# Kernel tuning notes

Measured on AMD Instinct MI355X. Metric: run time of the kernel, lower is better.

The kernel has to match this reference:

```python
import jax, jax.numpy as jnp
import numpy as np

CV_CHAN = 49  # displacement channels; radius = (CV_CHAN - 1) // 2 = 24


def conv1x1(x, W, b):
    # x: [B,C,H,Wd], W: [O,C], b: [O] -> [B,O,H,Wd]
    return jnp.einsum('oc,bchw->bohw', W, x) + b[None, :, None, None]


def corr_volume(f1, f2, radius, eps):
    """Shift-and-dot correlation along width. f1,f2: [B,C,H,W] -> [B,2r+1,H,W].
    Channel k corresponds to displacement d = k - radius; out-of-range positions are 0
    (handled by zero-padding, matching the torch zero-filled shifted tensors)."""
    f1n = f1 / (jnp.linalg.norm(f1, axis=1, keepdims=True) + eps)
    f2n = f2 / (jnp.linalg.norm(f2, axis=1, keepdims=True) + eps)
    Wd = f1.shape[3]
    pad = jnp.pad(f2n, ((0, 0), (0, 0), (0, 0), (radius, radius)))
    # shifted_k[x] = f2n[x - d] = pad[x + 2*radius - k]
    slices = [
        jnp.sum(f1n * jax.lax.dynamic_slice_in_dim(pad, 2 * radius - k, Wd, axis=3), axis=1)
        for k in range(2 * radius + 1)
    ]
    return jnp.stack(slices, axis=1)


def setup_inputs() -> dict:
    key = jax.random.key(0)
    ks = jax.random.split(key, 10)
    B, C, H, W = 4, 128, 128, 256
    F = 128  # fmap channels
    G = 96   # geo encoder output channels
    s = 0.05
    return {
        'feat_l1': jax.random.normal(ks[0], (B, C, H, W), jnp.float32),
        'feat_r1': jax.random.normal(ks[1], (B, C, H, W), jnp.float32),
        'cv0': jax.random.normal(ks[2], (B, CV_CHAN, H, W), jnp.float32),
        'cv1': jax.random.normal(ks[3], (B, CV_CHAN, H, W), jnp.float32),
        'cv2': jax.random.normal(ks[4], (B, CV_CHAN, H, W), jnp.float32),
        'W_f1': jax.random.normal(ks[5], (F, C), jnp.float32) * s,
        'b_f1': jnp.zeros((F,), jnp.float32),
        'W_f2': jax.random.normal(ks[6], (F, C), jnp.float32) * s,
        'b_f2': jnp.zeros((F,), jnp.float32),
        'W_geo': jax.random.normal(ks[7], (G, CV_CHAN), jnp.float32) * s,
        'b_geo': jnp.zeros((G,), jnp.float32),
        'W_sel': jax.random.normal(ks[8], (3, 3 * G), jnp.float32) * s,
        'b_sel': jnp.zeros((3,), jnp.float32),
    }


def reference(feat_l1, feat_r1, cv0, cv1, cv2,
              W_f1, b_f1, W_f2, b_f2, W_geo, b_geo, W_sel, b_sel):
    # init feature maps (init_fmap1 / init_fmap2 as 1x1 convs)
    fmap1 = conv1x1(feat_l1, W_f1, b_f1)
    fmap2 = conv1x1(feat_r1, W_f2, b_f2)
    radius = (CV_CHAN - 1) // 2
    init_corr = corr_volume(fmap1, fmap2, radius, 1e-8)  # [B, CV_CHAN, H, W]

    # geo_volume2 (1x1 conv CV_CHAN -> 96) applied to each geometric volume
    g0 = conv1x1(cv0, W_geo, b_geo)
    g1 = conv1x1(cv1, W_geo, b_geo)
    g2 = conv1x1(cv2, W_geo, b_geo)
    combined_g = jnp.concatenate([g0, g1, g2], axis=1)  # [B, 288, H, W]

    logits = conv1x1(combined_g, W_sel, b_sel)           # [B, 3, H, W]
    w = jax.nn.softmax(logits, axis=1)

    weighted = (w[:, 0:1] * cv0[:, :CV_CHAN]
                + w[:, 1:2] * cv1[:, :CV_CHAN]
                + w[:, 2:3] * cv2[:, :CV_CHAN])
    final = init_corr + weighted
    return (final, init_corr, w)
```

## Files before the change

kernel.cpp:

```cpp
#include <hip/hip_runtime.h>

#define HW 32768
#define WIDTH 256

typedef float f32x4 __attribute__((ext_vector_type(4)));
typedef short s16x8 __attribute__((ext_vector_type(8)));

__device__ __forceinline__ unsigned short f2bf(float f){
    unsigned int u = __float_as_uint(f);
    u += 0x7FFFu + ((u >> 16) & 1u);
    return (unsigned short)(u >> 16);
}
__device__ __forceinline__ unsigned int pk2(float a, float b){
    return (unsigned int)f2bf(a) | ((unsigned int)f2bf(b) << 16);
}

__global__ void k_pre(const float* __restrict__ W1, const float* __restrict__ W2,
                      unsigned int* __restrict__ Wb,
                      const float* __restrict__ Wsel, const float* __restrict__ bsel,
                      const float* __restrict__ Wgeo, const float* __restrict__ bgeo,
                      float* __restrict__ M, float* __restrict__ c0)
{
    if (blockIdx.x < 64){
        const int pi = blockIdx.x * 256 + threadIdx.x;
        const int j2   = pi & 3;
        const int l15  = (pi >> 2) & 15;
        const int quad = (pi >> 6) & 3;
        const int m    = (pi >> 8) & 7;
        const int kk   = (pi >> 11) & 3;
        const int F    = (pi >> 13) & 1;
        const float* Wm = F ? W2 : W1;
        const int row = m * 16 + l15;
        const int ch  = kk * 32 + quad * 8 + j2 * 2;
        Wb[pi] = pk2(Wm[row * 128 + ch], Wm[row * 128 + ch + 1]);
    } else {
        for (int u = threadIdx.x; u < 444; u += 256){
            if (u < 441){
                int s = u / 147; int r = u % 147; int i = r / 49; int k = r % 49;
                float acc = 0.f;
                for (int o = 0; o < 96; ++o)
                    acc += Wsel[s * 288 + i * 96 + o] * Wgeo[o * 49 + k];
                M[u] = acc;
            } else {
                int s = u - 441;
                float acc = bsel[s];
                for (int i = 0; i < 3; ++i)
                    for (int o = 0; o < 96; ++o)
                        acc += Wsel[s * 288 + i * 96 + o] * bgeo[o];
                c0[s] = acc;
            }
        }
    }
}

__global__ __launch_bounds__(256, 2) void k_fused(
    const float* __restrict__ fl, const float* __restrict__ fr,
    const unsigned int* __restrict__ Wbu,
    const float* __restrict__ b1, const float* __restrict__ b2,
    const float* __restrict__ cv0, const float* __restrict__ cv1,
    const float* __restrict__ cv2,
    const float* __restrict__ Mg, const float* __restrict__ c0g,
    float* __restrict__ icO, float* __restrict__ finalO, float* __restrict__ wO)
{
    __shared__ __align__(16) char pool[67584];
    __shared__ float s1[256], s2[256];
    __shared__ float Ms[441];
    __shared__ float c0s[3];
    unsigned short* f2s = (unsigned short*)pool;
    float* G            = (float*)pool;

    const int blk  = blockIdx.x;
    const int b    = blk >> 7;
    const int h    = blk & 127;
    const int tid  = threadIdx.x;
    const int wv   = tid >> 6;
    const int lane = tid & 63;
    const int quad = lane >> 4;
    const int l15  = lane & 15;

    for (int i = tid; i < 441; i += 256) Ms[i] = Mg[i];
    if (tid < 3) c0s[tid] = c0g[tid];

    const float* feats[2] = { fl + (size_t)b * 128 * HW + h * WIDTH,
                              fr + (size_t)b * 128 * HW + h * WIDTH };
    const float* bss[2]   = { b1, b2 };

    unsigned int f1p[64];

    #pragma unroll 1
    for (int Fi = 0; Fi < 2; ++Fi){
        const int F = 1 - Fi;
        const float* featB = feats[F];
        const float* bias  = bss[F];
        const unsigned int* WbF = Wbu + F * 8192;

        f32x4 acc[8][4];
        #pragma unroll
        for (int m = 0; m < 8; ++m)
            #pragma unroll
            for (int nt = 0; nt < 4; ++nt)
                acc[m][nt] = (f32x4){0.f, 0.f, 0.f, 0.f};

        float buf[3][8];
        #pragma unroll
        for (int t = 0; t < 2; ++t){
            const float* bp = featB + (size_t)(quad * 8) * HW + wv * 64 + t * 16 + l15;
            #pragma unroll
            for (int j = 0; j < 8; ++j) buf[t][j] = bp[(size_t)j * HW];
        }

        #pragma unroll
        for (int kk = 0; kk < 4; ++kk){
            s16x8 af[8];
            #pragma unroll
            for (int m = 0; m < 8; ++m)
                af[m] = *(const s16x8*)&WbF[(((kk * 8 + m) * 4 + quad) * 16 + l15) * 4];

            #pragma unroll
            for (int nt = 0; nt < 4; ++nt){
                const int t = kk * 4 + nt;
                if (t + 2 < 16){
                    const int kk2 = (t + 2) >> 2, nt2 = (t + 2) & 3;
                    const float* bp = featB + (size_t)(kk2 * 32 + quad * 8) * HW
                                      + wv * 64 + nt2 * 16 + l15;
                    #pragma unroll
                    for (int j = 0; j < 8; ++j) buf[(t + 2) % 3][j] = bp[(size_t)j * HW];
                }
                const float* cur = buf[t % 3];
                union { unsigned int u[4]; s16x8 v; } rb;
                rb.u[0] = pk2(cur[0], cur[1]); rb.u[1] = pk2(cur[2], cur[3]);
                rb.u[2] = pk2(cur[4], cur[5]); rb.u[3] = pk2(cur[6], cur[7]);
                #pragma unroll
                for (int m = 0; m < 8; ++m)
                    acc[m][nt] = __builtin_amdgcn_mfma_f32_16x16x32_bf16(af[m], rb.v, acc[m][nt], 0, 0, 0);
            }
        }

        float inv[4];
        #pragma unroll
        for (int nt = 0; nt < 4; ++nt){
            #pragma unroll
            for (int m = 0; m < 8; ++m)
                acc[m][nt] += *(const f32x4*)(bias + m * 16 + quad * 4);
            float n2 = 0.f;
            #pragma unroll
            for (int m = 0; m < 8; ++m)
                #pragma unroll
                for (int r = 0; r < 4; ++r)
                    n2 += acc[m][nt][r] * acc[m][nt][r];
            n2 += __shfl_xor(n2, 16, 64);
            n2 += __shfl_xor(n2, 32, 64);
            inv[nt] = 1.f / (sqrtf(n2) + 1e-8f);
        }

        if (F == 1){
            if (quad == 0){
                #pragma unroll
                for (int nt = 0; nt < 4; ++nt) s2[wv * 64 + nt * 16 + l15] = inv[nt];
            }
            #pragma unroll
            for (int nt = 0; nt < 4; ++nt){
                const int px = wv * 64 + nt * 16 + l15;
                #pragma unroll
                for (int m = 0; m < 8; ++m){
                    uint2 p;
                    p.x = pk2(acc[m][nt][0], acc[m][nt][1]);
                    p.y = pk2(acc[m][nt][2], acc[m][nt][3]);
                    *(uint2*)&f2s[px * 132 + m * 16 + quad * 4] = p;
                }
            }
        } else {
            #pragma unroll
            for (int m = 0; m < 8; ++m)
                #pragma unroll
                for (int nt = 0; nt < 4; ++nt){
                    f1p[m * 8 + nt * 2 + 0] = pk2(acc[m][nt][0], acc[m][nt][1]);
                    f1p[m * 8 + nt * 2 + 1] = pk2(acc[m][nt][2], acc[m][nt][3]);
                }
            if (quad == 0){
                #pragma unroll
                for (int nt = 0; nt < 4; ++nt) s1[wv * 64 + nt * 16 + l15] = inv[nt];
            }
        }
    }
    __syncthreads();

    f32x4 acc_c[4][4];
    #pragma unroll
    for (int st = 0; st < 4; ++st)
        #pragma unroll
        for (int ct = 0; ct < 4; ++ct)
            acc_c[st][ct] = (f32x4){0.f, 0.f, 0.f, 0.f};

    #pragma unroll
    for (int st = 0; st < 4; ++st){
        s16x8 afc[4];
        #pragma unroll
        for (int kk = 0; kk < 4; ++kk){
            union { unsigned int u[4]; s16x8 v; } r;
            #pragma unroll
            for (int j2 = 0; j2 < 4; ++j2){
                const int rp  = j2 & 1;
                const int qs  = (quad & 1) * 2 + (j2 >> 1);
                const int src = qs * 16 + l15;
                unsigned int a0 = (unsigned int)__shfl((int)f1p[(kk * 2 + 0) * 8 + st * 2 + rp], src, 64);
                unsigned int a1 = (unsigned int)__shfl((int)f1p[(kk * 2 + 1) * 8 + st * 2 + rp], src, 64);
                r.u[j2] = (quad >> 1) ? a1 : a0;
            }
            afc[kk] = r.v;
        }
        #pragma unroll
        for (int ct = 0; ct < 4; ++ct){
            const int s = wv * 64 + st * 16 + ct * 16 + l15 - 24;
            const bool valid = (s >= 0) && (s < WIDTH);
            const int sc = valid ? s : 0;
            #pragma unroll
            for (int kk = 0; kk < 4; ++kk){
                union { uint2 q2[2]; s16x8 v; } rb;
                rb.q2[0] = *(const uint2*)&f2s[sc * 132 + kk * 32 + quad * 8];
                rb.q2[1] = *(const uint2*)&f2s[sc * 132 + kk * 32 + quad * 8 + 4];
                s16x8 bf = rb.v;
                if (!valid) bf = (s16x8){0,0,0,0,0,0,0,0};
                acc_c[st][ct] = __builtin_amdgcn_mfma_f32_16x16x32_bf16(afc[kk], bf, acc_c[st][ct], 0, 0, 0);
            }
        }
    }
    __syncthreads();
    #pragma unroll
    for (int st = 0; st < 4; ++st)
        #pragma unroll
        for (int ct = 0; ct < 4; ++ct)
            #pragma unroll
            for (int r = 0; r < 4; ++r)
                G[((wv * 4 + st) * 16 + quad * 4 + r) * 66 + ct * 16 + l15] = acc_c[st][ct][r];
    __syncthreads();

    const int px = tid;
    const float sc1 = s1[px];
    const float* Gp = &G[px * 66 + (px & 15) + 48];
    const size_t rowoff = (size_t)h * WIDTH + px;
    const size_t cvbase = (size_t)b * 49 * HW + rowoff;
    float* icb = icO    + cvbase;
    float* fnb = finalO + cvbase;
    const float* c0p = cv0 + cvbase;
    const float* c1p = cv1 + cvbase;
    const float* c2p = cv2 + cvbase;

    float lg0 = c0s[0], lg1 = c0s[1], lg2 = c0s[2];
    #pragma unroll 7
    for (int dd = 0; dd < 49; ++dd){
        int s2i = px + 24 - dd;
        s2i = s2i < 0 ? 0 : (s2i > 255 ? 255 : s2i);
        const float icv = Gp[-dd] * sc1 * s2[s2i];
        icb[(size_t)dd * HW] = icv;
        const float a0 = c0p[(size_t)dd * HW];
        const float a1 = c1p[(size_t)dd * HW];
        const float a2 = c2p[(size_t)dd * HW];
        lg0 += Ms[dd]       * a0 + Ms[49  + dd] * a1 + Ms[98  + dd] * a2;
        lg1 += Ms[147 + dd] * a0 + Ms[196 + dd] * a1 + Ms[245 + dd] * a2;
        lg2 += Ms[294 + dd] * a0 + Ms[343 + dd] * a1 + Ms[392 + dd] * a2;
    }

    const float mx = fmaxf(lg0, fmaxf(lg1, lg2));
    const float e0 = expf(lg0 - mx), e1 = expf(lg1 - mx), e2 = expf(lg2 - mx);
    const float einv = 1.f / (e0 + e1 + e2);
    const float w0 = e0 * einv, w1 = e1 * einv, w2 = e2 * einv;

    float* wb = wO + (size_t)b * 3 * HW + rowoff;
    wb[0]      = w0;
    wb[HW]     = w1;
    wb[2 * HW] = w2;

    #pragma unroll 7
    for (int dd = 0; dd < 49; ++dd){
        int s2i = px + 24 - dd;
        s2i = s2i < 0 ? 0 : (s2i > 255 ? 255 : s2i);
        const float icv = Gp[-dd] * sc1 * s2[s2i];
        fnb[(size_t)dd * HW] = icv + w0 * c0p[(size_t)dd * HW]
                                   + w1 * c1p[(size_t)dd * HW]
                                   + w2 * c2p[(size_t)dd * HW];
    }
}

extern "C" void kernel_launch(void* const* d_in, const int* in_sizes, int n_in,
                              void* d_out, int out_size, void* d_ws, size_t ws_size,
                              hipStream_t stream)
{
    const float* feat_l1 = (const float*)d_in[0];
    const float* feat_r1 = (const float*)d_in[1];
    const float* cv0     = (const float*)d_in[2];
    const float* cv1     = (const float*)d_in[3];
    const float* cv2     = (const float*)d_in[4];
    const float* W_f1    = (const float*)d_in[5];
    const float* b_f1    = (const float*)d_in[6];
    const float* W_f2    = (const float*)d_in[7];
    const float* b_f2    = (const float*)d_in[8];
    const float* W_geo   = (const float*)d_in[9];
    const float* b_geo   = (const float*)d_in[10];
    const float* W_sel   = (const float*)d_in[11];
    const float* b_sel   = (const float*)d_in[12];

    float* finalO = (float*)d_out;
    float* icO    = (float*)d_out + 6422528;
    float* wO     = (float*)d_out + 12845056;

    unsigned int* Wb = (unsigned int*)d_ws;
    float* Mbuf  = (float*)((char*)d_ws + 65536);
    float* c0buf = Mbuf + 441;

    k_pre<<<65, 256, 0, stream>>>(W_f1, W_f2, Wb, W_sel, b_sel, W_geo, b_geo, Mbuf, c0buf);
    k_fused<<<512, 256, 0, stream>>>(feat_l1, feat_r1, Wb, b_f1, b_f2,
                                     cv0, cv1, cv2, Mbuf, c0buf,
                                     icO, finalO, wO);
}
```

Before: 274.9 us.

## Double threads per block, halve per-wave pixel tiles and split displacement loop

Launches 512 threads per row block instead of 256, so each wave handles 32 pixels instead of 64 in the projection and correlation MFMA stages, cutting accumulator and packed-feature register use. The epilogue splits the 49 displacement channels across two thread halves, reduces the partial softmax logits through shared memory, then broadcasts the weights back. The aim is more waves in flight to hide the latency of the bandwidth-heavy cv loads and output stores. It adds two extra block barriers and a small shared-memory buffer, and the per-wave weight fragment loads are now amortised over fewer MFMAs.

```diff
diff --git a/kernel.cpp b/kernel.cpp
--- a/kernel.cpp
+++ b/kernel.cpp
@@ -53,7 +53,7 @@
     }
 }
 
-__global__ __launch_bounds__(256, 2) void k_fused(
+__global__ __launch_bounds__(512, 4) void k_fused(
     const float* __restrict__ fl, const float* __restrict__ fr,
     const unsigned int* __restrict__ Wbu,
     const float* __restrict__ b1, const float* __restrict__ b2,
@@ -66,6 +66,7 @@
     __shared__ float s1[256], s2[256];
     __shared__ float Ms[441];
     __shared__ float c0s[3];
+    __shared__ float lgp[3][512];
     unsigned short* f2s = (unsigned short*)pool;
     float* G            = (float*)pool;
 
@@ -78,14 +79,14 @@
     const int quad = lane >> 4;
     const int l15  = lane & 15;
 
-    for (int i = tid; i < 441; i += 256) Ms[i] = Mg[i];
+    for (int i = tid; i < 441; i += 512) Ms[i] = Mg[i];
     if (tid < 3) c0s[tid] = c0g[tid];
 
     const float* feats[2] = { fl + (size_t)b * 128 * HW + h * WIDTH,
                               fr + (size_t)b * 128 * HW + h * WIDTH };
     const float* bss[2]   = { b1, b2 };
 
-    unsigned int f1p[64];
+    unsigned int f1p[32];
 
     #pragma unroll 1
     for (int Fi = 0; Fi < 2; ++Fi){
@@ -94,51 +95,49 @@
         const float* bias  = bss[F];
         const unsigned int* WbF = Wbu + F * 8192;
 
-        f32x4 acc[8][4];
+        f32x4 acc[8][2];
         #pragma unroll
         for (int m = 0; m < 8; ++m)
             #pragma unroll
-            for (int nt = 0; nt < 4; ++nt)
+            for (int nt = 0; nt < 2; ++nt)
                 acc[m][nt] = (f32x4){0.f, 0.f, 0.f, 0.f};
 
         float buf[3][8];
         #pragma unroll
         for (int t = 0; t < 2; ++t){
-            const float* bp = featB + (size_t)(quad * 8) * HW + wv * 64 + t * 16 + l15;
+            const float* bp = featB + (size_t)(quad * 8) * HW + wv * 32 + t * 16 + l15;
             #pragma unroll
             for (int j = 0; j < 8; ++j) buf[t][j] = bp[(size_t)j * HW];
         }
 
         #pragma unroll
         for (int kk = 0; kk < 4; ++kk){
-            s16x8 af[8];
-            #pragma unroll
-            for (int m = 0; m < 8; ++m)
-                af[m] = *(const s16x8*)&WbF[(((kk * 8 + m) * 4 + quad) * 16 + l15) * 4];
-
-            #pragma unroll
-            for (int nt = 0; nt < 4; ++nt){
-                const int t = kk * 4 + nt;
-                if (t + 2 < 16){
-                    const int kk2 = (t + 2) >> 2, nt2 = (t + 2) & 3;
+            union { unsigned int u[4]; s16x8 v; } rb[2];
+            #pragma unroll
+            for (int nt = 0; nt < 2; ++nt){
+                const int t = kk * 2 + nt;
+                if (t + 2 < 8){
+                    const int kk2 = (t + 2) >> 1, nt2 = (t + 2) & 1;
                     const float* bp = featB + (size_t)(kk2 * 32 + quad * 8) * HW
-                                      + wv * 64 + nt2 * 16 + l15;
+                                      + wv * 32 + nt2 * 16 + l15;
                     #pragma unroll
                     for (int j = 0; j < 8; ++j) buf[(t + 2) % 3][j] = bp[(size_t)j * HW];
                 }
                 const float* cur = buf[t % 3];
-                union { unsigned int u[4]; s16x8 v; } rb;
-                rb.u[0] = pk2(cur[0], cur[1]); rb.u[1] = pk2(cur[2], cur[3]);
-                rb.u[2] = pk2(cur[4], cur[5]); rb.u[3] = pk2(cur[6], cur[7]);
-                #pragma unroll
-                for (int m = 0; m < 8; ++m)
-                    acc[m][nt] = __builtin_amdgcn_mfma_f32_16x16x32_bf16(af[m], rb.v, acc[m][nt], 0, 0, 0);
-            }
-        }
-
-        float inv[4];
-        #pragma unroll
-        for (int nt = 0; nt < 4; ++nt){
+                rb[nt].u[0] = pk2(cur[0], cur[1]); rb[nt].u[1] = pk2(cur[2], cur[3]);
+                rb[nt].u[2] = pk2(cur[4], cur[5]); rb[nt].u[3] = pk2(cur[6], cur[7]);
+            }
+            #pragma unroll
+            for (int m = 0; m < 8; ++m){
+                const s16x8 af = *(const s16x8*)&WbF[(((kk * 8 + m) * 4 + quad) * 16 + l15) * 4];
+                acc[m][0] = __builtin_amdgcn_mfma_f32_16x16x32_bf16(af, rb[0].v, acc[m][0], 0, 0, 0);
+                acc[m][1] = __builtin_amdgcn_mfma_f32_16x16x32_bf16(af, rb[1].v, acc[m][1], 0, 0, 0);
+            }
+        }
+
+        float inv[2];
+        #pragma unroll
+        for (int nt = 0; nt < 2; ++nt){
             #pragma unroll
             for (int m = 0; m < 8; ++m)
                 acc[m][nt] += *(const f32x4*)(bias + m * 16 + quad * 4);
@@ -156,11 +155,11 @@
         if (F == 1){
             if (quad == 0){
                 #pragma unroll
-                for (int nt = 0; nt < 4; ++nt) s2[wv * 64 + nt * 16 + l15] = inv[nt];
-            }
-            #pragma unroll
-            for (int nt = 0; nt < 4; ++nt){
-                const int px = wv * 64 + nt * 16 + l15;
+                for (int nt = 0; nt < 2; ++nt) s2[wv * 32 + nt * 16 + l15] = inv[nt];
+            }
+            #pragma unroll
+            for (int nt = 0; nt < 2; ++nt){
+                const int px = wv * 32 + nt * 16 + l15;
                 #pragma unroll
                 for (int m = 0; m < 8; ++m){
                     uint2 p;
@@ -173,27 +172,27 @@
             #pragma unroll
             for (int m = 0; m < 8; ++m)
                 #pragma unroll
-                for (int nt = 0; nt < 4; ++nt){
-                    f1p[m * 8 + nt * 2 + 0] = pk2(acc[m][nt][0], acc[m][nt][1]);
-                    f1p[m * 8 + nt * 2 + 1] = pk2(acc[m][nt][2], acc[m][nt][3]);
+                for (int nt = 0; nt < 2; ++nt){
+                    f1p[m * 4 + nt * 2 + 0] = pk2(acc[m][nt][0], acc[m][nt][1]);
+                    f1p[m * 4 + nt * 2 + 1] = pk2(acc[m][nt][2], acc[m][nt][3]);
                 }
             if (quad == 0){
                 #pragma unroll
-                for (int nt = 0; nt < 4; ++nt) s1[wv * 64 + nt * 16 + l15] = inv[nt];
-            }
-        }
-    }
-    __syncthreads();
-
-    f32x4 acc_c[4][4];
+                for (int nt = 0; nt < 2; ++nt) s1[wv * 32 + nt * 16 + l15] = inv[nt];
+            }
+        }
+    }
+    __syncthreads();
+
+    f32x4 acc_c[2][4];
     #pragma unroll
-    for (int st = 0; st < 4; ++st)
+    for (int st = 0; st < 2; ++st)
         #pragma unroll
         for (int ct = 0; ct < 4; ++ct)
             acc_c[st][ct] = (f32x4){0.f, 0.f, 0.f, 0.f};
 
     #pragma unroll
-    for (int st = 0; st < 4; ++st){
+    for (int st = 0; st < 2; ++st){
         s16x8 afc[4];
         #pragma unroll
         for (int kk = 0; kk < 4; ++kk){
@@ -203,15 +202,15 @@
                 const int rp  = j2 & 1;
                 const int qs  = (quad & 1) * 2 + (j2 >> 1);
                 const int src = qs * 16 + l15;
-                unsigned int a0 = (unsigned int)__shfl((int)f1p[(kk * 2 + 0) * 8 + st * 2 + rp], src, 64);
-                unsigned int a1 = (unsigned int)__shfl((int)f1p[(kk * 2 + 1) * 8 + st * 2 + rp], src, 64);
+                unsigned int a0 = (unsigned int)__shfl((int)f1p[(kk * 2 + 0) * 4 + st * 2 + rp], src, 64);
+                unsigned int a1 = (unsigned int)__shfl((int)f1p[(kk * 2 + 1) * 4 + st * 2 + rp], src, 64);
                 r.u[j2] = (quad >> 1) ? a1 : a0;
             }
             afc[kk] = r.v;
         }
         #pragma unroll
         for (int ct = 0; ct < 4; ++ct){
-            const int s = wv * 64 + st * 16 + ct * 16 + l15 - 24;
+            const int s = wv * 32 + st * 16 + ct * 16 + l15 - 24;
             const bool valid = (s >= 0) && (s < WIDTH);
             const int sc = valid ? s : 0;
             #pragma unroll
@@ -227,15 +226,16 @@
     }
     __syncthreads();
     #pragma unroll
-    for (int st = 0; st < 4; ++st)
+    for (int st = 0; st < 2; ++st)
         #pragma unroll
         for (int ct = 0; ct < 4; ++ct)
             #pragma unroll
             for (int r = 0; r < 4; ++r)
-                G[((wv * 4 + st) * 16 + quad * 4 + r) * 66 + ct * 16 + l15] = acc_c[st][ct][r];
-    __syncthreads();
-
-    const int px = tid;
+                G[((wv * 2 + st) * 16 + quad * 4 + r) * 66 + ct * 16 + l15] = acc_c[st][ct][r];
+    __syncthreads();
+
+    const int px   = tid & 255;
+    const int half = tid >> 8;
     const float sc1 = s1[px];
     const float* Gp = &G[px * 66 + (px & 15) + 48];
     const size_t rowoff = (size_t)h * WIDTH + px;
@@ -246,39 +246,56 @@
     const float* c1p = cv1 + cvbase;
     const float* c2p = cv2 + cvbase;
 
-    float lg0 = c0s[0], lg1 = c0s[1], lg2 = c0s[2];
-    #pragma unroll 7
-    for (int dd = 0; dd < 49; ++dd){
-        int s2i = px + 24 - dd;
-        s2i = s2i < 0 ? 0 : (s2i > 255 ? 255 : s2i);
-        const float icv = Gp[-dd] * sc1 * s2[s2i];
-        icb[(size_t)dd * HW] = icv;
-        const float a0 = c0p[(size_t)dd * HW];
-        const float a1 = c1p[(size_t)dd * HW];
-        const float a2 = c2p[(size_t)dd * HW];
-        lg0 += Ms[dd]       * a0 + Ms[49  + dd] * a1 + Ms[98  + dd] * a2;
-        lg1 += Ms[147 + dd] * a0 + Ms[196 + dd] * a1 + Ms[245 + dd] * a2;
-        lg2 += Ms[294 + dd] * a0 + Ms[343 + dd] * a1 + Ms[392 + dd] * a2;
-    }
-
-    const float mx = fmaxf(lg0, fmaxf(lg1, lg2));
-    const float e0 = expf(lg0 - mx), e1 = expf(lg1 - mx), e2 = expf(lg2 - mx);
-    const float einv = 1.f / (e0 + e1 + e2);
-    const float w0 = e0 * einv, w1 = e1 * einv, w2 = e2 * einv;
-
-    float* wb = wO + (size_t)b * 3 * HW + rowoff;
-    wb[0]      = w0;
-    wb[HW]     = w1;
-    wb[2 * HW] = w2;
-
-    #pragma unroll 7
-    for (int dd = 0; dd < 49; ++dd){
-        int s2i = px + 24 - dd;
-        s2i = s2i < 0 ? 0 : (s2i > 255 ? 255 : s2i);
-        const float icv = Gp[-dd] * sc1 * s2[s2i];
-        fnb[(size_t)dd * HW] = icv + w0 * c0p[(size_t)dd * HW]
-                                   + w1 * c1p[(size_t)dd * HW]
-                                   + w2 * c2p[(size_t)dd * HW];
+    const int dd0 = half * 25;
+
+    float lg0 = 0.f, lg1 = 0.f, lg2 = 0.f;
+    #pragma unroll 5
+    for (int i = 0; i < 25; ++i){
+        const int dd = dd0 + i;
+        if (dd < 49){
+            int s2i = px + 24 - dd;
+            s2i = s2i < 0 ? 0 : (s2i > 255 ? 255 : s2i);
+            const float icv = Gp[-dd] * sc1 * s2[s2i];
+            icb[(size_t)dd * HW] = icv;
+            const float a0 = c0p[(size_t)dd * HW];
+            const float a1 = c1p[(size_t)dd * HW];
+            const float a2 = c2p[(size_t)dd * HW];
+            lg0 += Ms[dd]       * a0 + Ms[49  + dd] * a1 + Ms[98  + dd] * a2;
+            lg1 += Ms[147 + dd] * a0 + Ms[196 + dd] * a1 + Ms[245 + dd] * a2;
+            lg2 += Ms[294 + dd] * a0 + Ms[343 + dd] * a1 + Ms[392 + dd] * a2;
+        }
+    }
+    lgp[0][tid] = lg0; lgp[1][tid] = lg1; lgp[2][tid] = lg2;
+    __syncthreads();
+
+    if (tid < 256){
+        const float L0 = c0s[0] + lgp[0][tid] + lgp[0][tid + 256];
+        const float L1 = c0s[1] + lgp[1][tid] + lgp[1][tid + 256];
+        const float L2 = c0s[2] + lgp[2][tid] + lgp[2][tid + 256];
+        const float mx = fmaxf(L0, fmaxf(L1, L2));
+        const float e0 = expf(L0 - mx), e1 = expf(L1 - mx), e2 = expf(L2 - mx);
+        const float einv = 1.f / (e0 + e1 + e2);
+        const float w0 = e0 * einv, w1 = e1 * einv, w2 = e2 * einv;
+        lgp[0][tid] = w0; lgp[1][tid] = w1; lgp[2][tid] = w2;
+        float* wb = wO + (size_t)b * 3 * HW + rowoff;
+        wb[0]      = w0;
+        wb[HW]     = w1;
+        wb[2 * HW] = w2;
+    }
+    __syncthreads();
+
+    const float w0 = lgp[0][px], w1 = lgp[1][px], w2 = lgp[2][px];
+    #pragma unroll 5
+    for (int i = 0; i < 25; ++i){
+        const int dd = dd0 + i;
+        if (dd < 49){
+            int s2i = px + 24 - dd;
+            s2i = s2i < 0 ? 0 : (s2i > 255 ? 255 : s2i);
+            const float icv = Gp[-dd] * sc1 * s2[s2i];
+            fnb[(size_t)dd * HW] = icv + w0 * c0p[(size_t)dd * HW]
+                                       + w1 * c1p[(size_t)dd * HW]
+                                       + w2 * c2p[(size_t)dd * HW];
+        }
     }
 }
 
@@ -309,7 +326,7 @@
     float* c0buf = Mbuf + 441;
 
     k_pre<<<65, 256, 0, stream>>>(W_f1, W_f2, Wb, W_sel, b_sel, W_geo, b_geo, Mbuf, c0buf);
-    k_fused<<<512, 256, 0, stream>>>(feat_l1, feat_r1, Wb, b_f1, b_f2,
+    k_fused<<<512, 512, 0, stream>>>(feat_l1, feat_r1, Wb, b_f1, b_f2,
                                      cv0, cv1, cv2, Mbuf, c0buf,
                                      icO, finalO, wO);
 }
```

New measurement: 285.8 us. 3.9% more time.

## Vectorize epilogue with 4-pixel float4 access, deepen prefetch, pad f2 LDS rows

Applied to the files above, without the earlier changes.

Reworks the epilogue so each thread handles 4 adjacent pixels and a quarter of the 49 displacement channels. The cv loads and output stores become 16-byte vectors, and partial logits are combined with cross-lane shuffles. The feature prefetch ring goes from 3 to 4 buffers. The f2 LDS row stride goes from 132 to 144 so the B operand can be read as one 128-bit load. The costs are more LDS (73.7 KB per block, which may threaten 2 blocks per CU), more registers, and stores that are now less coalesced across threads within a channel.

```diff
diff --git a/kernel.cpp b/kernel.cpp
--- a/kernel.cpp
+++ b/kernel.cpp
@@ -62,7 +62,7 @@
     const float* __restrict__ Mg, const float* __restrict__ c0g,
     float* __restrict__ icO, float* __restrict__ finalO, float* __restrict__ wO)
 {
-    __shared__ __align__(16) char pool[67584];
+    __shared__ __align__(16) char pool[73728];
     __shared__ float s1[256], s2[256];
     __shared__ float Ms[441];
     __shared__ float c0s[3];
@@ -101,9 +101,9 @@
             for (int nt = 0; nt < 4; ++nt)
                 acc[m][nt] = (f32x4){0.f, 0.f, 0.f, 0.f};
 
-        float buf[3][8];
-        #pragma unroll
-        for (int t = 0; t < 2; ++t){
+        float buf[4][8];
+        #pragma unroll
+        for (int t = 0; t < 3; ++t){
             const float* bp = featB + (size_t)(quad * 8) * HW + wv * 64 + t * 16 + l15;
             #pragma unroll
             for (int j = 0; j < 8; ++j) buf[t][j] = bp[(size_t)j * HW];
@@ -119,14 +119,14 @@
             #pragma unroll
             for (int nt = 0; nt < 4; ++nt){
                 const int t = kk * 4 + nt;
-                if (t + 2 < 16){
-                    const int kk2 = (t + 2) >> 2, nt2 = (t + 2) & 3;
+                if (t + 3 < 16){
+                    const int kk2 = (t + 3) >> 2, nt2 = (t + 3) & 3;
                     const float* bp = featB + (size_t)(kk2 * 32 + quad * 8) * HW
                                       + wv * 64 + nt2 * 16 + l15;
                     #pragma unroll
-                    for (int j = 0; j < 8; ++j) buf[(t + 2) % 3][j] = bp[(size_t)j * HW];
+                    for (int j = 0; j < 8; ++j) buf[(t + 3) & 3][j] = bp[(size_t)j * HW];
                 }
-                const float* cur = buf[t % 3];
+                const float* cur = buf[t & 3];
                 union { unsigned int u[4]; s16x8 v; } rb;
                 rb.u[0] = pk2(cur[0], cur[1]); rb.u[1] = pk2(cur[2], cur[3]);
                 rb.u[2] = pk2(cur[4], cur[5]); rb.u[3] = pk2(cur[6], cur[7]);
@@ -166,7 +166,7 @@
                     uint2 p;
                     p.x = pk2(acc[m][nt][0], acc[m][nt][1]);
                     p.y = pk2(acc[m][nt][2], acc[m][nt][3]);
-                    *(uint2*)&f2s[px * 132 + m * 16 + quad * 4] = p;
+                    *(uint2*)&f2s[px * 144 + m * 16 + quad * 4] = p;
                 }
             }
         } else {
@@ -216,10 +216,7 @@
             const int sc = valid ? s : 0;
             #pragma unroll
             for (int kk = 0; kk < 4; ++kk){
-                union { uint2 q2[2]; s16x8 v; } rb;
-                rb.q2[0] = *(const uint2*)&f2s[sc * 132 + kk * 32 + quad * 8];
-                rb.q2[1] = *(const uint2*)&f2s[sc * 132 + kk * 32 + quad * 8 + 4];
-                s16x8 bf = rb.v;
+                s16x8 bf = *(const s16x8*)&f2s[sc * 144 + kk * 32 + quad * 8];
                 if (!valid) bf = (s16x8){0,0,0,0,0,0,0,0};
                 acc_c[st][ct] = __builtin_amdgcn_mfma_f32_16x16x32_bf16(afc[kk], bf, acc_c[st][ct], 0, 0, 0);
             }
@@ -235,10 +232,10 @@
                 G[((wv * 4 + st) * 16 + quad * 4 + r) * 66 + ct * 16 + l15] = acc_c[st][ct][r];
     __syncthreads();
 
-    const int px = tid;
-    const float sc1 = s1[px];
-    const float* Gp = &G[px * 66 + (px & 15) + 48];
-    const size_t rowoff = (size_t)h * WIDTH + px;
+    const int g   = tid >> 2;
+    const int sl  = tid & 3;
+    const int px0 = g * 4;
+    const size_t rowoff = (size_t)h * WIDTH + px0;
     const size_t cvbase = (size_t)b * 49 * HW + rowoff;
     float* icb = icO    + cvbase;
     float* fnb = finalO + cvbase;
@@ -246,39 +243,73 @@
     const float* c1p = cv1 + cvbase;
     const float* c2p = cv2 + cvbase;
 
-    float lg0 = c0s[0], lg1 = c0s[1], lg2 = c0s[2];
-    #pragma unroll 7
-    for (int dd = 0; dd < 49; ++dd){
-        int s2i = px + 24 - dd;
-        s2i = s2i < 0 ? 0 : (s2i > 255 ? 255 : s2i);
-        const float icv = Gp[-dd] * sc1 * s2[s2i];
-        icb[(size_t)dd * HW] = icv;
-        const float a0 = c0p[(size_t)dd * HW];
-        const float a1 = c1p[(size_t)dd * HW];
-        const float a2 = c2p[(size_t)dd * HW];
-        lg0 += Ms[dd]       * a0 + Ms[49  + dd] * a1 + Ms[98  + dd] * a2;
-        lg1 += Ms[147 + dd] * a0 + Ms[196 + dd] * a1 + Ms[245 + dd] * a2;
-        lg2 += Ms[294 + dd] * a0 + Ms[343 + dd] * a1 + Ms[392 + dd] * a2;
-    }
-
-    const float mx = fmaxf(lg0, fmaxf(lg1, lg2));
-    const float e0 = expf(lg0 - mx), e1 = expf(lg1 - mx), e2 = expf(lg2 - mx);
-    const float einv = 1.f / (e0 + e1 + e2);
-    const float w0 = e0 * einv, w1 = e1 * einv, w2 = e2 * einv;
-
-    float* wb = wO + (size_t)b * 3 * HW + rowoff;
-    wb[0]      = w0;
-    wb[HW]     = w1;
-    wb[2 * HW] = w2;
-
-    #pragma unroll 7
-    for (int dd = 0; dd < 49; ++dd){
-        int s2i = px + 24 - dd;
-        s2i = s2i < 0 ? 0 : (s2i > 255 ? 255 : s2i);
-        const float icv = Gp[-dd] * sc1 * s2[s2i];
-        fnb[(size_t)dd * HW] = icv + w0 * c0p[(size_t)dd * HW]
-                                   + w1 * c1p[(size_t)dd * HW]
-                                   + w2 * c2p[(size_t)dd * HW];
+    f32x4 lg0 = (f32x4){0.f,0.f,0.f,0.f};
+    f32x4 lg1 = (f32x4){0.f,0.f,0.f,0.f};
+    f32x4 lg2 = (f32x4){0.f,0.f,0.f,0.f};
+    #pragma unroll
+    for (int i = 0; i < 13; ++i){
+        const int dd = sl * 13 + i;
+        if (dd < 49){
+            const f32x4 a0 = *(const f32x4*)(c0p + (size_t)dd * HW);
+            const f32x4 a1 = *(const f32x4*)(c1p + (size_t)dd * HW);
+            const f32x4 a2 = *(const f32x4*)(c2p + (size_t)dd * HW);
+            const float m00 = Ms[dd],       m01 = Ms[49  + dd], m02 = Ms[98  + dd];
+            const float m10 = Ms[147 + dd], m11 = Ms[196 + dd], m12 = Ms[245 + dd];
+            const float m20 = Ms[294 + dd], m21 = Ms[343 + dd], m22 = Ms[392 + dd];
+            #pragma unroll
+            for (int p = 0; p < 4; ++p){
+                lg0[p] += m00 * a0[p] + m01 * a1[p] + m02 * a2[p];
+                lg1[p] += m10 * a0[p] + m11 * a1[p] + m12 * a2[p];
+                lg2[p] += m20 * a0[p] + m21 * a1[p] + m22 * a2[p];
+            }
+        }
+    }
+    #pragma unroll
+    for (int p = 0; p < 4; ++p){
+        lg0[p] += __shfl_xor(lg0[p], 1, 64); lg0[p] += __shfl_xor(lg0[p], 2, 64);
+        lg1[p] += __shfl_xor(lg1[p], 1, 64); lg1[p] += __shfl_xor(lg1[p], 2, 64);
+        lg2[p] += __shfl_xor(lg2[p], 1, 64); lg2[p] += __shfl_xor(lg2[p], 2, 64);
+    }
+
+    f32x4 w0v, w1v, w2v;
+    #pragma unroll
+    for (int p = 0; p < 4; ++p){
+        const float L0 = c0s[0] + lg0[p];
+        const float L1 = c0s[1] + lg1[p];
+        const float L2 = c0s[2] + lg2[p];
+        const float mx = fmaxf(L0, fmaxf(L1, L2));
+        const float e0 = expf(L0 - mx), e1 = expf(L1 - mx), e2 = expf(L2 - mx);
+        const float einv = 1.f / (e0 + e1 + e2);
+        w0v[p] = e0 * einv; w1v[p] = e1 * einv; w2v[p] = e2 * einv;
+    }
+    if (sl == 0){
+        float* wb = wO + (size_t)b * 3 * HW + rowoff;
+        *(f32x4*)(wb)          = w0v;
+        *(f32x4*)(wb + HW)     = w1v;
+        *(f32x4*)(wb + 2 * HW) = w2v;
+    }
+
+    const f32x4 s1v = *(const f32x4*)&s1[px0];
+
+    #pragma unroll
+    for (int i = 0; i < 13; ++i){
+        const int dd = sl * 13 + i;
+        if (dd < 49){
+            const f32x4 a0 = *(const f32x4*)(c0p + (size_t)dd * HW);
+            const f32x4 a1 = *(const f32x4*)(c1p + (size_t)dd * HW);
+            const f32x4 a2 = *(const f32x4*)(c2p + (size_t)dd * HW);
+            f32x4 icv, fv;
+            #pragma unroll
+            for (int p = 0; p < 4; ++p){
+                const int px = px0 + p;
+                int s2i = px + 24 - dd;
+                s2i = s2i < 0 ? 0 : (s2i > 255 ? 255 : s2i);
+                icv[p] = G[px * 66 + (px & 15) + 48 - dd] * s1v[p] * s2[s2i];
+                fv[p]  = icv[p] + w0v[p] * a0[p] + w1v[p] * a1[p] + w2v[p] * a2[p];
+            }
+            *(f32x4*)(icb + (size_t)dd * HW) = icv;
+            *(f32x4*)(fnb + (size_t)dd * HW) = fv;
+        }
     }
 }
 
```

New measurement: 284.3 us. +3.4%, slower.
